# Optimization experiments

Hardware: AMD Instinct MI355X
Metric: run time of the kernel (lower is better)

The kernel has to match this reference:

```python
import jax, jax.numpy as jnp
import numpy as np

BN_EPS = 1e-5


def gcn_conv(x, src, dst, n, W, b):
    # PyG GCNConv: h = x @ W; add self-loops; symmetric deg^{-1/2} norm; scatter-add; + bias
    h = x @ W
    sl = jnp.arange(n, dtype=src.dtype)
    src_f = jnp.concatenate([src, sl])
    dst_f = jnp.concatenate([dst, sl])
    deg = jax.ops.segment_sum(jnp.ones_like(dst_f, dtype=h.dtype), dst_f, num_segments=n)
    dis = jnp.where(deg > 0, jax.lax.rsqrt(jnp.maximum(deg, 1.0)), 0.0)
    norm = dis[src_f] * dis[dst_f]                       # [E+N]
    msg = h[src_f] * norm[:, None]                       # gather + scale
    out = jax.ops.segment_sum(msg, dst_f, num_segments=n)  # scatter-add
    return out + b


def batchnorm(x, g, b):
    # training-mode BatchNorm1d (batch statistics), deterministic
    mu = jnp.mean(x, axis=0)
    var = jnp.mean((x - mu) ** 2, axis=0)
    return g * (x - mu) * jax.lax.rsqrt(var + BN_EPS) + b


def setup_inputs() -> dict:
    key = jax.random.key(0)
    ks = jax.random.split(key, 12)
    N, E, F_IN, D, M, G = 40000, 640000, 128, 128, 256, 2000
    x = jax.random.normal(ks[0], (N, F_IN), dtype=jnp.float32)
    edge_index = jax.random.randint(ks[1], (2, E), 0, N, dtype=jnp.int64)
    batch = jnp.sort(jax.random.randint(ks[2], (N,), 0, G, dtype=jnp.int64))
    s = lambda fi: 1.0 / np.sqrt(fi)
    W1 = jax.random.normal(ks[3], (F_IN, D), dtype=jnp.float32) * s(F_IN)
    b1 = jnp.zeros((D,), jnp.float32)
    W2 = jax.random.normal(ks[4], (D, D), dtype=jnp.float32) * s(D)
    b2 = jnp.zeros((D,), jnp.float32)
    bn1_g = jnp.ones((D,), jnp.float32); bn1_b = jnp.zeros((D,), jnp.float32)
    bn2_g = jnp.ones((D,), jnp.float32); bn2_b = jnp.zeros((D,), jnp.float32)
    fc1_w = jax.random.normal(ks[5], (D, M), dtype=jnp.float32) * s(D)
    fc1_b = jnp.zeros((M,), jnp.float32)
    fc2_w = jax.random.normal(ks[6], (M, M), dtype=jnp.float32) * s(M)
    fc2_b = jnp.zeros((M,), jnp.float32)
    fc3_w = jax.random.normal(ks[7], (M, 1), dtype=jnp.float32) * s(M)
    fc3_b = jnp.zeros((1,), jnp.float32)
    return dict(x=x, edge_index=edge_index, batch=batch, num_graphs=G,
                W1=W1, b1=b1, W2=W2, b2=b2,
                bn1_g=bn1_g, bn1_b=bn1_b, bn2_g=bn2_g, bn2_b=bn2_b,
                fc1_w=fc1_w, fc1_b=fc1_b, fc2_w=fc2_w, fc2_b=fc2_b,
                fc3_w=fc3_w, fc3_b=fc3_b)


def reference(x, edge_index, batch, num_graphs, W1, b1, W2, b2,
              bn1_g, bn1_b, bn2_g, bn2_b,
              fc1_w, fc1_b, fc2_w, fc2_b, fc3_w, fc3_b):
    n = x.shape[0]
    src, dst = edge_index[0], edge_index[1]
    h = gcn_conv(x, src, dst, n, W1, b1)
    h = jax.nn.relu(batchnorm(h, bn1_g, bn1_b))
    h = gcn_conv(h, src, dst, n, W2, b2)
    h = jax.nn.relu(batchnorm(h, bn2_g, bn2_b))
    g = jax.ops.segment_sum(h, batch, num_segments=num_graphs)  # scatter_sum pooling [G, D]
    g = jax.nn.relu(g @ fc1_w + fc1_b)   # dropout is identity in eval
    g = jax.nn.relu(g @ fc2_w + fc2_b)
    return g @ fc3_w + fc3_b             # [G, 1]
```

## Files before the change

### kernel.cpp

```cpp
#include <hip/hip_runtime.h>
#include <hip/hip_fp16.h>

#define NN 40000
#define NE 640000
#define DF 128
#define NG 2000
#define NCH 157
#define FILLB 625
#define G1_BLKS 313
#define G2_BLKS 625
#define NCHUNK 64
#define ECH 10000
#define NOCT 8
#define QN 5120
#define NPAD (NOCT * QN)
#define NWIN 160
#define HISTB (NCHUNK * NOCT)

typedef unsigned int u32;
typedef __attribute__((ext_vector_type(8))) short short8;
typedef __attribute__((ext_vector_type(4))) float floatx4;

__device__ inline float2 bf2_to_f2(u32 u) {
    return make_float2(__uint_as_float(u << 16), __uint_as_float(u & 0xffff0000u));
}
__device__ inline u32 f_to_bf(float f) {
    u32 u = __float_as_uint(f);
    return (u + 0x7fffu + ((u >> 16) & 1u)) >> 16;
}
__device__ inline u32 pack_bf2(float a, float b) {
    return f_to_bf(a) | (f_to_bf(b) << 16);
}
__device__ inline float bf_to_f(short s) {
    return __uint_as_float(((u32)(unsigned short)s) << 16);
}
__device__ inline float colw_to_f(int cw) {
    return __half2float(__ushort_as_half((unsigned short)((u32)cw >> 16)));
}

template<bool BF16IN, bool FUSE_BN, bool WT_F32, bool TILE128>
__device__ __forceinline__ void gemm_core(const void* __restrict__ Xv, const void* __restrict__ wsrc,
                                          u32* __restrict__ outb, const float* __restrict__ slots,
                                          const float* __restrict__ gam, const float* __restrict__ bet,
                                          int bid, char* sbuf, float* sc, float* sh) {
    unsigned short* wlds = (unsigned short*)sbuf;
    unsigned short* clds = (unsigned short*)sbuf;
    int tid = threadIdx.x;
    int row0 = bid * (TILE128 ? 128 : 64);

    if (FUSE_BN) {
        if (tid < 128) {
            float s = 0.f, q = 0.f;
            for (int k = 0; k < 64; k++) {
                s += slots[k * 256 + tid];
                q += slots[k * 256 + 128 + tid];
            }
            const float inv_n = 1.0f / (float)NN;
            float mu = s * inv_n;
            float va = fmaf(-mu, mu, q * inv_n);
            float a = gam[tid] * rsqrtf(va + 1e-5f);
            sc[tid] = a;
            sh[tid] = fmaf(-mu, a, bet[tid]);
        }
    }
    if (WT_F32) {
        const float* W = (const float*)wsrc;
        for (int i = tid; i < 16384; i += 256) {
            int k = i >> 7, c = i & 127;
            wlds[c * 136 + k] = (unsigned short)f_to_bf(W[i]);
        }
    } else {
        const unsigned short* wt = (const unsigned short*)wsrc;
        for (int i = tid; i < 2048; i += 256) {
            int c = i >> 4, s = i & 15;
            *(uint4*)&wlds[c * 136 + s * 8] = ((const uint4*)wt)[i];
        }
    }
    __syncthreads();

    int lane = tid & 63;
    int wave = tid >> 6;
    int qr = lane >> 4;
    int rl = lane & 15;

    if (TILE128) {
        int rA0 = row0 + wave * 32 + rl;
        int rA1 = rA0 + 16;
        int rA0c = rA0 < NN ? rA0 : NN - 1;
        int rA1c = rA1 < NN ? rA1 : NN - 1;
        floatx4 acc[2][8];
#pragma unroll
        for (int a = 0; a < 2; a++)
#pragma unroll
            for (int b = 0; b < 8; b++) acc[a][b] = (floatx4){0.f, 0.f, 0.f, 0.f};
#pragma unroll
        for (int kb = 0; kb < 4; kb++) {
            int k0 = kb * 32 + qr * 8;
            short8 a0, a1;
            if (!BF16IN) {
                const float* p0 = (const float*)Xv + (size_t)rA0c * DF + k0;
                const float* p1 = (const float*)Xv + (size_t)rA1c * DF + k0;
                float4 u0 = *(const float4*)p0, u1 = *(const float4*)(p0 + 4);
                float4 v0 = *(const float4*)p1, v1 = *(const float4*)(p1 + 4);
                float fa[8] = {u0.x, u0.y, u0.z, u0.w, u1.x, u1.y, u1.z, u1.w};
                float fb[8] = {v0.x, v0.y, v0.z, v0.w, v1.x, v1.y, v1.z, v1.w};
#pragma unroll
                for (int j = 0; j < 8; j++) { a0[j] = (short)f_to_bf(fa[j]); a1[j] = (short)f_to_bf(fb[j]); }
            } else {
                a0 = *(const short8*)((const u32*)Xv + (size_t)rA0c * 64 + (k0 >> 1));
                a1 = *(const short8*)((const u32*)Xv + (size_t)rA1c * 64 + (k0 >> 1));
                if (FUSE_BN) {
#pragma unroll
                    for (int j = 0; j < 8; j++) {
                        float f0 = fmaxf(fmaf(bf_to_f(a0[j]), sc[k0 + j], sh[k0 + j]), 0.f);
                        float f1 = fmaxf(fmaf(bf_to_f(a1[j]), sc[k0 + j], sh[k0 + j]), 0.f);
                        a0[j] = (short)f_to_bf(f0);
                        a1[j] = (short)f_to_bf(f1);
                    }
                }
            }
#pragma unroll
            for (int ct = 0; ct < 8; ct++) {
                short8 bfr = *(const short8*)&wlds[(ct * 16 + rl) * 136 + k0];
                acc[0][ct] = __builtin_amdgcn_mfma_f32_16x16x32_bf16(a0, bfr, acc[0][ct], 0, 0, 0);
                acc[1][ct] = __builtin_amdgcn_mfma_f32_16x16x32_bf16(a1, bfr, acc[1][ct], 0, 0, 0);
            }
        }
        __syncthreads();
#pragma unroll
        for (int rt = 0; rt < 2; rt++)
#pragma unroll
            for (int ct = 0; ct < 8; ct++)
#pragma unroll
                for (int r = 0; r < 4; r++) {
                    int lr = wave * 32 + rt * 16 + qr * 4 + r;
                    int c = ct * 16 + rl;
                    clds[lr * 136 + c] = (unsigned short)f_to_bf(acc[rt][ct][r]);
                }
        __syncthreads();
        for (int i = tid; i < 2048; i += 256) {
            int lr = i >> 4, s = i & 15;
            int grow = row0 + lr;
            if (grow < NN) {
                uint4 v = *(const uint4*)&clds[lr * 136 + s * 8];
                ((uint4*)(outb + (size_t)grow * 64))[s] = v;
            }
        }
    } else {
        int rA = row0 + wave * 16 + rl;
        floatx4 acc[8];
#pragma unroll
        for (int b = 0; b < 8; b++) acc[b] = (floatx4){0.f, 0.f, 0.f, 0.f};
#pragma unroll
        for (int kb = 0; kb < 4; kb++) {
            int k0 = kb * 32 + qr * 8;
            short8 a0;
            if (!BF16IN) {
                const float* p0 = (const float*)Xv + (size_t)rA * DF + k0;
                float4 u0 = *(const float4*)p0, u1 = *(const float4*)(p0 + 4);
                float fa[8] = {u0.x, u0.y, u0.z, u0.w, u1.x, u1.y, u1.z, u1.w};
#pragma unroll
                for (int j = 0; j < 8; j++) a0[j] = (short)f_to_bf(fa[j]);
            } else {
                a0 = *(const short8*)((const u32*)Xv + (size_t)rA * 64 + (k0 >> 1));
                if (FUSE_BN) {
#pragma unroll
                    for (int j = 0; j < 8; j++) {
                        float f0 = fmaxf(fmaf(bf_to_f(a0[j]), sc[k0 + j], sh[k0 + j]), 0.f);
                        a0[j] = (short)f_to_bf(f0);
                    }
                }
            }
#pragma unroll
            for (int ct = 0; ct < 8; ct++) {
                short8 bfr = *(const short8*)&wlds[(ct * 16 + rl) * 136 + k0];
                acc[ct] = __builtin_amdgcn_mfma_f32_16x16x32_bf16(a0, bfr, acc[ct], 0, 0, 0);
            }
        }
        __syncthreads();
#pragma unroll
        for (int ct = 0; ct < 8; ct++)
#pragma unroll
            for (int r = 0; r < 4; r++) {
                int lr = wave * 16 + qr * 4 + r;
                int c = ct * 16 + rl;
                clds[lr * 136 + c] = (unsigned short)f_to_bf(acc[ct][r]);
            }
        __syncthreads();
        for (int i = tid; i < 1024; i += 256) {
            int lr = i >> 4, s = i & 15;
            uint4 v = *(const uint4*)&clds[lr * 136 + s * 8];
            ((uint4*)(outb + (size_t)(row0 + lr) * 64))[s] = v;
        }
    }
}

__global__ __launch_bounds__(256, 4) void k_countgemm(const int* __restrict__ dst,
                                                      int* __restrict__ degT, int* __restrict__ rank,
                                                      int* __restrict__ wsum, float* __restrict__ slots0,
                                                      const float* __restrict__ W1, const float* __restrict__ W2,
                                                      unsigned short* __restrict__ wt2,
                                                      const float* __restrict__ X, u32* __restrict__ outb) {
    __shared__ __align__(16) char sbuf[34816];
    __shared__ float sc[128], sh[128];
    int bid = blockIdx.x;
    int tid = threadIdx.x;
    if (bid < HISTB) {
        int c = bid >> 3, oct = bid & 7;
        int nlo = oct * QN;
        int* hist = (int*)sbuf;
        for (int i = tid; i < QN; i += 256) hist[i] = 0;
        __syncthreads();
        int ebase = c * ECH;
        for (int i = tid; i < ECH; i += 256) {
            int d = dst[ebase + i];
            int t = d - nlo;
            if ((u32)t < (u32)QN) rank[ebase + i] = atomicAdd(&hist[t], 1);
        }
        __syncthreads();
        for (int i = tid; i < QN; i += 256) degT[(size_t)c * NPAD + nlo + i] = hist[i];
        int wv = tid >> 6, lane = tid & 63;
        for (int lw = wv; lw < 20; lw += 4) {
            int v = hist[lw * 256 + lane] + hist[lw * 256 + 64 + lane]
                  + hist[lw * 256 + 128 + lane] + hist[lw * 256 + 192 + lane];
            for (int off = 32; off > 0; off >>= 1) v += __shfl_down(v, off);
            if (lane == 0) wsum[c * NWIN + oct * 20 + lw] = v;
        }
        return;
    }
    if (bid < HISTB + 2) {
        float* s = slots0 + (size_t)(bid - HISTB) * 64 * 256;
        for (int i = tid; i < 64 * 256; i += 256) s[i] = 0.f;
        return;
    }
    if (bid == HISTB + 2) {
        for (int i = tid; i < 128 * 128; i += 256) {
            int k = i >> 7, cc = i & 127;
            wt2[cc * 128 + k] = (unsigned short)f_to_bf(W2[i]);
        }
        return;
    }
    gemm_core<false, false, true, true>(X, W1, outb, nullptr, nullptr, nullptr,
                                        bid - HISTB - 3, sbuf, sc, sh);
}

__global__ __launch_bounds__(256) void k_scan(const int* __restrict__ degT, const int* __restrict__ wsum,
                                              int* __restrict__ baseT,
                                              int* __restrict__ row_ptr, float* __restrict__ dis) {
    __shared__ int red[256];
    __shared__ int ls[256];
    int tid = threadIdx.x;
    int wnd = blockIdx.x;
    int part = 0;
    for (int idx = tid; idx < NCHUNK * NWIN; idx += 256) {
        int wp = idx % NWIN;
        if (wp < wnd) part += wsum[idx];
    }
    red[tid] = part;
    int n = wnd * 256 + tid;
    int run = 0;
#pragma unroll 4
    for (int c = 0; c < NCHUNK; c++) {
        int v = degT[(size_t)c * NPAD + n];
        baseT[(size_t)c * NPAD + n] = run;
        run += v;
    }
    int d = run;
    ls[tid] = d;
    __syncthreads();
#pragma unroll
    for (int off = 128; off > 0; off >>= 1) {
        if (tid < off) red[tid] += red[tid + off];
        __syncthreads();
    }
    int base = red[0];
#pragma unroll
    for (int off = 1; off < 256; off <<= 1) {
        int t = (tid >= off) ? ls[tid - off] : 0;
        __syncthreads();
        ls[tid] += t;
        __syncthreads();
    }
    if (n < NN) {
        int r = base + ls[tid] - d;
        row_ptr[n] = r;
        dis[n] = rsqrtf((float)(d + 1));
    }
    if (wnd == NCH - 1 && tid == 0) row_ptr[NN] = NE;
}

__global__ __launch_bounds__(256) void k_fill(const int* __restrict__ src, const int* __restrict__ dst,
                                              const int* __restrict__ rank, const int* __restrict__ row_ptr,
                                              const int* __restrict__ baseT,
                                              const float* __restrict__ dis, u32* __restrict__ col) {
    int e0 = blockIdx.x * 1024 + threadIdx.x;
#pragma unroll
    for (int q = 0; q < 4; q++) {
        int e = e0 + q * 256;
        int d = dst[e];
        int s = src[e];
        int r = rank[e];
        int c = e / ECH;
        u32 h = (u32)__half_as_ushort(__float2half(dis[s]));
        col[row_ptr[d] + baseT[(size_t)c * NPAD + d] + r] = (u32)s | (h << 16);
    }
}

__global__ __launch_bounds__(256, 4) void k_gemm2(const u32* __restrict__ Hb, const unsigned short* __restrict__ wt2,
                                                  u32* __restrict__ outb, const float* __restrict__ slots,
                                                  const float* __restrict__ gam, const float* __restrict__ bet) {
    __shared__ __align__(16) char sbuf[34816];
    __shared__ float sc[128], sh[128];
    gemm_core<true, true, false, false>(Hb, wt2, outb, slots, gam, bet, blockIdx.x, sbuf, sc, sh);
}

__global__ __launch_bounds__(256) void k_gather(const u32* __restrict__ Hb, const int* __restrict__ row_ptr,
                                                const u32* __restrict__ col, const float* __restrict__ dis,
                                                const float* __restrict__ bias, u32* __restrict__ outb,
                                                float* __restrict__ slots) {
    __shared__ float sred[4][128];
    __shared__ float qred[4][128];
    int t = threadIdx.x & 63;
    int wv = threadIdx.x >> 6;
    int node = blockIdx.x * 4 + wv;
    float di = dis[node];
    float2 acc;
    {
        float2 a = bf2_to_f2(Hb[(size_t)node * 64 + t]);
        float s = di * di;
        acc = make_float2(a.x * s, a.y * s);
    }
    int lo = row_ptr[node], hi = row_ptr[node + 1];
    for (int base = lo; base < hi; base += 64) {
        int m = hi - base; if (m > 64) m = 64;
        int cw = 0;
        if (t < m) cw = (int)col[base + t];
        int j = 0;
        for (; j + 8 <= m; j += 8) {
            int c0 = __shfl(cw, j),     c1 = __shfl(cw, j + 1);
            int c2 = __shfl(cw, j + 2), c3 = __shfl(cw, j + 3);
            int c4 = __shfl(cw, j + 4), c5 = __shfl(cw, j + 5);
            int c6 = __shfl(cw, j + 6), c7 = __shfl(cw, j + 7);
            u32 u0 = Hb[(size_t)(c0 & 0xffff) * 64 + t], u1 = Hb[(size_t)(c1 & 0xffff) * 64 + t];
            u32 u2 = Hb[(size_t)(c2 & 0xffff) * 64 + t], u3 = Hb[(size_t)(c3 & 0xffff) * 64 + t];
            u32 u4 = Hb[(size_t)(c4 & 0xffff) * 64 + t], u5 = Hb[(size_t)(c5 & 0xffff) * 64 + t];
            u32 u6 = Hb[(size_t)(c6 & 0xffff) * 64 + t], u7 = Hb[(size_t)(c7 & 0xffff) * 64 + t];
            float w0 = di * colw_to_f(c0), w1 = di * colw_to_f(c1);
            float w2 = di * colw_to_f(c2), w3 = di * colw_to_f(c3);
            float w4 = di * colw_to_f(c4), w5 = di * colw_to_f(c5);
            float w6 = di * colw_to_f(c6), w7 = di * colw_to_f(c7);
            float2 h0 = bf2_to_f2(u0), h1 = bf2_to_f2(u1), h2 = bf2_to_f2(u2), h3 = bf2_to_f2(u3);
            float2 h4 = bf2_to_f2(u4), h5 = bf2_to_f2(u5), h6 = bf2_to_f2(u6), h7 = bf2_to_f2(u7);
            acc.x = fmaf(h3.x, w3, fmaf(h2.x, w2, fmaf(h1.x, w1, fmaf(h0.x, w0, acc.x))));
            acc.y = fmaf(h3.y, w3, fmaf(h2.y, w2, fmaf(h1.y, w1, fmaf(h0.y, w0, acc.y))));
            acc.x = fmaf(h7.x, w7, fmaf(h6.x, w6, fmaf(h5.x, w5, fmaf(h4.x, w4, acc.x))));
            acc.y = fmaf(h7.y, w7, fmaf(h6.y, w6, fmaf(h5.y, w5, fmaf(h4.y, w4, acc.y))));
        }
        for (; j < m; j++) {
            int c0 = __shfl(cw, j);
            float w0 = di * colw_to_f(c0);
            float2 h0 = bf2_to_f2(Hb[(size_t)(c0 & 0xffff) * 64 + t]);
            acc.x = fmaf(h0.x, w0, acc.x);
            acc.y = fmaf(h0.y, w0, acc.y);
        }
    }
    float2 b = ((const float2*)bias)[t];
    acc.x += b.x; acc.y += b.y;
    outb[(size_t)node * 64 + t] = pack_bf2(acc.x, acc.y);
    sred[wv][2 * t] = acc.x;     sred[wv][2 * t + 1] = acc.y;
    qred[wv][2 * t] = acc.x * acc.x; qred[wv][2 * t + 1] = acc.y * acc.y;
    __syncthreads();
    int tid = threadIdx.x;
    if (tid < 128) {
        float s = sred[0][tid] + sred[1][tid] + sred[2][tid] + sred[3][tid];
        float q = qred[0][tid] + qred[1][tid] + qred[2][tid] + qred[3][tid];
        int slot = blockIdx.x & 63;
        atomicAdd(&slots[slot * 256 + tid], s);
        atomicAdd(&slots[slot * 256 + 128 + tid], q);
    }
}

__global__ __launch_bounds__(256) void k_poolfc(const u32* __restrict__ Hb, const int* __restrict__ batch,
                                                const float* __restrict__ slots,
                                                const float* __restrict__ gam, const float* __restrict__ bet,
                                                const float* __restrict__ fc1w, const float* __restrict__ fc1b,
                                                const float* __restrict__ fc2w, const float* __restrict__ fc2b,
                                                const float* __restrict__ fc3w, const float* __restrict__ fc3b,
                                                float* __restrict__ out) {
    __shared__ float sc[128], sh[128];
    __shared__ float pooled[4][128];
    __shared__ float g1[4][256];
    __shared__ float g2[4][256];
    __shared__ int bnds[5];
    int tid = threadIdx.x;
    int gbase = blockIdx.x * 4;
    if (tid < 128) {
        float s = 0.f, q = 0.f;
        for (int k = 0; k < 64; k++) {
            s += slots[k * 256 + tid];
            q += slots[k * 256 + 128 + tid];
        }
        const float inv_n = 1.0f / (float)NN;
        float mu = s * inv_n;
        float va = fmaf(-mu, mu, q * inv_n);
        float a = gam[tid] * rsqrtf(va + 1e-5f);
        sc[tid] = a;
        sh[tid] = fmaf(-mu, a, bet[tid]);
    } else if (tid < 133) {
        int target = gbase + (tid - 128);
        int a = 0, b = NN;
        while (a < b) { int m = (a + b) >> 1; if (batch[m] < target) a = m + 1; else b = m; }
        bnds[tid - 128] = a;
    }
    __syncthreads();
    {
        int g = tid >> 6, p = tid & 63;
        int lo = bnds[g], hi = bnds[g + 1];
        float a0 = 0.f, a1 = 0.f;
        float sc0 = sc[2 * p], sh0 = sh[2 * p], sc1 = sc[2 * p + 1], sh1 = sh[2 * p + 1];
        for (int i = lo; i < hi; i++) {
            float2 v = bf2_to_f2(Hb[(size_t)i * 64 + p]);
            a0 += fmaxf(fmaf(v.x, sc0, sh0), 0.f);
            a1 += fmaxf(fmaf(v.y, sc1, sh1), 0.f);
        }
        pooled[g][2 * p] = a0;
        pooled[g][2 * p + 1] = a1;
    }
    __syncthreads();
    {
        float x0 = 0.f, x1 = 0.f, x2 = 0.f, x3 = 0.f;
        for (int k = 0; k < 128; k++) {
            float wv = fc1w[k * 256 + tid];
            x0 = fmaf(pooled[0][k], wv, x0);
            x1 = fmaf(pooled[1][k], wv, x1);
            x2 = fmaf(pooled[2][k], wv, x2);
            x3 = fmaf(pooled[3][k], wv, x3);
        }
        float bb = fc1b[tid];
        g1[0][tid] = fmaxf(x0 + bb, 0.f);
        g1[1][tid] = fmaxf(x1 + bb, 0.f);
        g1[2][tid] = fmaxf(x2 + bb, 0.f);
        g1[3][tid] = fmaxf(x3 + bb, 0.f);
    }
    __syncthreads();
    {
        float x0 = 0.f, x1 = 0.f, x2 = 0.f, x3 = 0.f;
        for (int k = 0; k < 256; k++) {
            float wv = fc2w[k * 256 + tid];
            x0 = fmaf(g1[0][k], wv, x0);
            x1 = fmaf(g1[1][k], wv, x1);
            x2 = fmaf(g1[2][k], wv, x2);
            x3 = fmaf(g1[3][k], wv, x3);
        }
        float bb = fc2b[tid];
        g2[0][tid] = fmaxf(x0 + bb, 0.f);
        g2[1][tid] = fmaxf(x1 + bb, 0.f);
        g2[2][tid] = fmaxf(x2 + bb, 0.f);
        g2[3][tid] = fmaxf(x3 + bb, 0.f);
    }
    __syncthreads();
    {
        int lane = tid & 63, wv = tid >> 6;
        float s = fmaf(g2[wv][lane], fc3w[lane],
                  fmaf(g2[wv][64 + lane], fc3w[64 + lane],
                  fmaf(g2[wv][128 + lane], fc3w[128 + lane],
                       g2[wv][192 + lane] * fc3w[192 + lane])));
        for (int off = 32; off > 0; off >>= 1) s += __shfl_down(s, off);
        if (lane == 0) out[gbase + wv] = s + fc3b[0];
    }
}

extern "C" void kernel_launch(void* const* d_in, const int* in_sizes, int n_in,
                              void* d_out, int out_size, void* d_ws, size_t ws_size,
                              hipStream_t stream) {
    const float* x    = (const float*)d_in[0];
    const int*   ei   = (const int*)d_in[1];
    const int*   batch= (const int*)d_in[2];
    const float* W1   = (const float*)d_in[4];
    const float* b1   = (const float*)d_in[5];
    const float* W2   = (const float*)d_in[6];
    const float* b2   = (const float*)d_in[7];
    const float* bn1g = (const float*)d_in[8];
    const float* bn1b = (const float*)d_in[9];
    const float* bn2g = (const float*)d_in[10];
    const float* bn2b = (const float*)d_in[11];
    const float* fc1w = (const float*)d_in[12];
    const float* fc1b = (const float*)d_in[13];
    const float* fc2w = (const float*)d_in[14];
    const float* fc2b = (const float*)d_in[15];
    const float* fc3w = (const float*)d_in[16];
    const float* fc3b = (const float*)d_in[17];
    const int* src = ei;
    const int* dst = ei + NE;
    float* outp = (float*)d_out;

    char* w = (char*)d_ws;
    size_t o = 0;
    auto alloc = [&](size_t bytes) -> char* {
        char* p = w + o;
        o = (o + bytes + 255) & ~(size_t)255;
        return p;
    };
    int*   degT    = (int*)alloc((size_t)NCHUNK * NPAD * 4);
    int*   baseT   = (int*)alloc((size_t)NCHUNK * NPAD * 4);
    int*   wsum    = (int*)alloc((size_t)NCHUNK * NWIN * 4);
    float* slots0  = (float*)alloc((size_t)2 * 64 * 256 * 4);
    int*   row_ptr = (int*)alloc((size_t)(NN + 1) * 4);
    int*   rank    = (int*)alloc((size_t)NE * 4);
    u32*   col     = (u32*)alloc((size_t)NE * 4);
    float* dis     = (float*)alloc((size_t)NN * 4);
    unsigned short* wt2 = (unsigned short*)alloc(128 * 128 * 2);
    u32*   bufA    = (u32*)alloc((size_t)NN * 64 * 4);
    u32*   bufB    = (u32*)alloc((size_t)NN * 64 * 4);
    float* slotsA  = slots0;
    float* slotsB  = slots0 + 64 * 256;

    k_countgemm<<<HISTB + 3 + G1_BLKS, 256, 0, stream>>>(dst, degT, rank, wsum, slots0,
                                                         W1, W2, wt2, x, bufA);
    k_scan<<<NCH, 256, 0, stream>>>(degT, wsum, baseT, row_ptr, dis);
    k_fill<<<FILLB, 256, 0, stream>>>(src, dst, rank, row_ptr, baseT, dis, col);
    k_gather<<<NN / 4, 256, 0, stream>>>(bufA, row_ptr, col, dis, b1, bufB, slotsA);
    k_gemm2<<<G2_BLKS, 256, 0, stream>>>(bufB, wt2, bufA, slotsA, bn1g, bn1b);
    k_gather<<<NN / 4, 256, 0, stream>>>(bufA, row_ptr, col, dis, b2, bufB, slotsB);
    k_poolfc<<<NG / 4, 256, 0, stream>>>(bufB, batch, slotsB, bn2g, bn2b,
                                         fc1w, fc1b, fc2w, fc2b, fc3w, fc3b, outp);
}
```

Before: 263.3 us.

## Software-pipeline gather loads, raise gather occupancy, retile gemm2, drop modulo in scan

The neighbour-gather loop is restructured into a 4-wide software pipeline: the next group of column indices and feature rows is loaded while the previous group is accumulated, with masked weights standing in for a remainder loop. k_gather gets a launch-bounds occupancy hint of 8 blocks per CU. k_gemm2 switches a template flag, apparently to larger 128-row tiles, and launches with the same block count as gemm1. k_scan replaces a per-iteration modulo with an incremental wrap counter. The pipelining is meant to hide gather memory latency, at the cost of extra registers and wasted dummy loads on short rows.

```diff
diff --git a/kernel.cpp b/kernel.cpp
--- a/kernel.cpp
+++ b/kernel.cpp
@@ -8,7 +8,6 @@
 #define NCH 157
 #define FILLB 625
 #define G1_BLKS 313
-#define G2_BLKS 625
 #define NCHUNK 64
 #define ECH 10000
 #define NOCT 8
@@ -252,9 +251,10 @@
     int tid = threadIdx.x;
     int wnd = blockIdx.x;
     int part = 0;
+    int wp = tid < NWIN ? tid : tid - NWIN;
     for (int idx = tid; idx < NCHUNK * NWIN; idx += 256) {
-        int wp = idx % NWIN;
         if (wp < wnd) part += wsum[idx];
+        wp += 96; if (wp >= NWIN) wp -= NWIN;
     }
     red[tid] = part;
     int n = wnd * 256 + tid;
@@ -311,57 +311,65 @@
                                                   const float* __restrict__ gam, const float* __restrict__ bet) {
     __shared__ __align__(16) char sbuf[34816];
     __shared__ float sc[128], sh[128];
-    gemm_core<true, true, false, false>(Hb, wt2, outb, slots, gam, bet, blockIdx.x, sbuf, sc, sh);
-}
-
-__global__ __launch_bounds__(256) void k_gather(const u32* __restrict__ Hb, const int* __restrict__ row_ptr,
-                                                const u32* __restrict__ col, const float* __restrict__ dis,
-                                                const float* __restrict__ bias, u32* __restrict__ outb,
-                                                float* __restrict__ slots) {
+    gemm_core<true, true, false, true>(Hb, wt2, outb, slots, gam, bet, blockIdx.x, sbuf, sc, sh);
+}
+
+__global__ __launch_bounds__(256, 8) void k_gather(const u32* __restrict__ Hb, const int* __restrict__ row_ptr,
+                                                   const u32* __restrict__ col, const float* __restrict__ dis,
+                                                   const float* __restrict__ bias, u32* __restrict__ outb,
+                                                   float* __restrict__ slots) {
     __shared__ float sred[4][128];
     __shared__ float qred[4][128];
     int t = threadIdx.x & 63;
     int wv = threadIdx.x >> 6;
     int node = blockIdx.x * 4 + wv;
     float di = dis[node];
+    int lo = row_ptr[node], hi = row_ptr[node + 1];
     float2 acc;
     {
         float2 a = bf2_to_f2(Hb[(size_t)node * 64 + t]);
         float s = di * di;
         acc = make_float2(a.x * s, a.y * s);
     }
-    int lo = row_ptr[node], hi = row_ptr[node + 1];
     for (int base = lo; base < hi; base += 64) {
         int m = hi - base; if (m > 64) m = 64;
         int cw = 0;
         if (t < m) cw = (int)col[base + t];
-        int j = 0;
-        for (; j + 8 <= m; j += 8) {
-            int c0 = __shfl(cw, j),     c1 = __shfl(cw, j + 1);
-            int c2 = __shfl(cw, j + 2), c3 = __shfl(cw, j + 3);
-            int c4 = __shfl(cw, j + 4), c5 = __shfl(cw, j + 5);
-            int c6 = __shfl(cw, j + 6), c7 = __shfl(cw, j + 7);
-            u32 u0 = Hb[(size_t)(c0 & 0xffff) * 64 + t], u1 = Hb[(size_t)(c1 & 0xffff) * 64 + t];
-            u32 u2 = Hb[(size_t)(c2 & 0xffff) * 64 + t], u3 = Hb[(size_t)(c3 & 0xffff) * 64 + t];
-            u32 u4 = Hb[(size_t)(c4 & 0xffff) * 64 + t], u5 = Hb[(size_t)(c5 & 0xffff) * 64 + t];
-            u32 u6 = Hb[(size_t)(c6 & 0xffff) * 64 + t], u7 = Hb[(size_t)(c7 & 0xffff) * 64 + t];
-            float w0 = di * colw_to_f(c0), w1 = di * colw_to_f(c1);
-            float w2 = di * colw_to_f(c2), w3 = di * colw_to_f(c3);
-            float w4 = di * colw_to_f(c4), w5 = di * colw_to_f(c5);
-            float w6 = di * colw_to_f(c6), w7 = di * colw_to_f(c7);
-            float2 h0 = bf2_to_f2(u0), h1 = bf2_to_f2(u1), h2 = bf2_to_f2(u2), h3 = bf2_to_f2(u3);
-            float2 h4 = bf2_to_f2(u4), h5 = bf2_to_f2(u5), h6 = bf2_to_f2(u6), h7 = bf2_to_f2(u7);
-            acc.x = fmaf(h3.x, w3, fmaf(h2.x, w2, fmaf(h1.x, w1, fmaf(h0.x, w0, acc.x))));
-            acc.y = fmaf(h3.y, w3, fmaf(h2.y, w2, fmaf(h1.y, w1, fmaf(h0.y, w0, acc.y))));
-            acc.x = fmaf(h7.x, w7, fmaf(h6.x, w6, fmaf(h5.x, w5, fmaf(h4.x, w4, acc.x))));
-            acc.y = fmaf(h7.y, w7, fmaf(h6.y, w6, fmaf(h5.y, w5, fmaf(h4.y, w4, acc.y))));
-        }
-        for (; j < m; j++) {
-            int c0 = __shfl(cw, j);
-            float w0 = di * colw_to_f(c0);
-            float2 h0 = bf2_to_f2(Hb[(size_t)(c0 & 0xffff) * 64 + t]);
-            acc.x = fmaf(h0.x, w0, acc.x);
-            acc.y = fmaf(h0.y, w0, acc.y);
+        int ng = (m + 3) >> 2;
+        int c[4]; u32 u[4];
+#pragma unroll
+        for (int q = 0; q < 4; q++) {
+            int idx = q < m ? q : 0;
+            c[q] = __shfl(cw, idx);
+            u[q] = Hb[(size_t)(c[q] & 0xffff) * 64 + t];
+        }
+        for (int g = 1; g < ng; g++) {
+            int c2[4]; u32 u2[4];
+#pragma unroll
+            for (int q = 0; q < 4; q++) {
+                int ii = g * 4 + q;
+                int idx = ii < m ? ii : 0;
+                c2[q] = __shfl(cw, idx);
+                u2[q] = Hb[(size_t)(c2[q] & 0xffff) * 64 + t];
+            }
+#pragma unroll
+            for (int q = 0; q < 4; q++) {
+                int ii = (g - 1) * 4 + q;
+                float wq = ii < m ? di * colw_to_f(c[q]) : 0.f;
+                float2 h = bf2_to_f2(u[q]);
+                acc.x = fmaf(h.x, wq, acc.x);
+                acc.y = fmaf(h.y, wq, acc.y);
+            }
+#pragma unroll
+            for (int q = 0; q < 4; q++) { c[q] = c2[q]; u[q] = u2[q]; }
+        }
+#pragma unroll
+        for (int q = 0; q < 4; q++) {
+            int ii = (ng - 1) * 4 + q;
+            float wq = ii < m ? di * colw_to_f(c[q]) : 0.f;
+            float2 h = bf2_to_f2(u[q]);
+            acc.x = fmaf(h.x, wq, acc.x);
+            acc.y = fmaf(h.y, wq, acc.y);
         }
     }
     float2 b = ((const float2*)bias)[t];
@@ -520,7 +528,7 @@
     k_scan<<<NCH, 256, 0, stream>>>(degT, wsum, baseT, row_ptr, dis);
     k_fill<<<FILLB, 256, 0, stream>>>(src, dst, rank, row_ptr, baseT, dis, col);
     k_gather<<<NN / 4, 256, 0, stream>>>(bufA, row_ptr, col, dis, b1, bufB, slotsA);
-    k_gemm2<<<G2_BLKS, 256, 0, stream>>>(bufB, wt2, bufA, slotsA, bn1g, bn1b);
+    k_gemm2<<<G1_BLKS, 256, 0, stream>>>(bufB, wt2, bufA, slotsA, bn1g, bn1b);
     k_gather<<<NN / 4, 256, 0, stream>>>(bufA, row_ptr, col, dis, b2, bufB, slotsB);
     k_poolfc<<<NG / 4, 256, 0, stream>>>(bufB, batch, slotsB, bn2g, bn2b,
                                          fc1w, fc1b, fc2w, fc2b, fc3w, fc3b, outp);
```

Result: no change. 261.6 us (-0.7%).
